# Performance work log

Hardware: AMD Instinct MI355X
Metric: run time of the kernel (lower is better)

## Reference

```python
import jax, jax.numpy as jnp
import numpy as np


def setup_inputs() -> dict:
    key = jax.random.key(0)
    ks = jax.random.split(key, 4)
    B, T, D, H = 128, 512, 256, 512
    scale = 1.0 / np.sqrt(D)
    return {
        "x": jax.random.normal(ks[0], (B, T, D), dtype=jnp.float32),
        "h0": jnp.zeros((B, H), dtype=jnp.float32),
        "kernelr": jax.random.normal(ks[1], (D, H), dtype=jnp.float32) * scale,
        "kernelz": jax.random.normal(ks[2], (D, H), dtype=jnp.float32) * scale,
        "kernelh": jax.random.normal(ks[3], (D, H), dtype=jnp.float32) * scale,
        "memoryr": jnp.ones((H,), dtype=jnp.float32),
        "memoryz": jnp.ones((H,), dtype=jnp.float32),
        "br": jnp.zeros((H,), dtype=jnp.float32),
        "bz": jnp.zeros((H,), dtype=jnp.float32),
    }


def reference(x, h0, kernelr, kernelz, kernelh, memoryr, memoryz, br, bz):
    # Precompute all input projections as one batched GEMM over (B*T, D).
    # xr/xz/xh: [T, B, H]
    xr = jnp.einsum("btd,dh->tbh", x, kernelr) + br
    xz = jnp.einsum("btd,dh->tbh", x, kernelz) + bz
    xh = jnp.einsum("btd,dh->tbh", x, kernelh)

    def step(h, inp):
        pr, pz, ph = inp
        r = jnp.tanh(pr + h * memoryr) + 1.0
        z = jax.nn.sigmoid(pz + h * memoryz)
        out = z * h + (1.0 - z) * jnp.tanh(ph + r * h)
        return out, out

    _, outs = jax.lax.scan(step, h0, (xr, xz, xh))  # outs: [T, B, H]
    return jnp.transpose(outs, (1, 0, 2))  # [B, T, H]
```

## Files before the change

kernel.cpp:

```cpp
#include <hip/hip_runtime.h>

typedef _Float16 f16;
typedef _Float16 f16x8 __attribute__((ext_vector_type(8)));
typedef _Float16 f16x4 __attribute__((ext_vector_type(4)));
typedef float f32x4 __attribute__((ext_vector_type(4)));

__device__ __forceinline__ float rcpf(float x) { return __builtin_amdgcn_rcpf(x); }

__global__ void __launch_bounds__(256) cvt_w(const float* __restrict__ Wr,
                                             const float* __restrict__ Wz,
                                             const float* __restrict__ Wh,
                                             f16* __restrict__ out) {
  int o = blockIdx.x * 256 + threadIdx.x;
  int rl = o & 15, ni = (o >> 4) & 3, kq = (o >> 6) & 3, kt = (o >> 8) & 7;
  int wnt = o >> 11;
  int w = wnt % 3, nt = wnt / 3;
  int n = nt * 64 + ni * 16 + rl;
  int k0 = kt * 32 + kq * 8;
  const float* W = (w == 0) ? Wr : ((w == 1) ? Wz : Wh);
  f16x8 v;
#pragma unroll
  for (int e = 0; e < 8; ++e) v[e] = (f16)W[(size_t)(k0 + e) * 512 + n];
  *(f16x8*)(out + (size_t)o * 8) = v;
}

__global__ void __launch_bounds__(256) cvt_x(const float* __restrict__ in,
                                             f16* __restrict__ out) {
  int o = blockIdx.x * 256 + threadIdx.x;
  int rl = o & 15, kq = (o >> 4) & 3, kt = (o >> 6) & 7, m16 = o >> 9;
  const float* src = in + (size_t)(m16 * 16 + rl) * 256 + kt * 32 + kq * 8;
  f16x8 v;
#pragma unroll
  for (int e = 0; e < 8; ++e) v[e] = (f16)src[e];
  *(f16x8*)(out + (size_t)o * 8) = v;
}

__global__ void __launch_bounds__(512, 4) brc_fused(
    const f16* __restrict__ Af, const f16* __restrict__ Bf,
    const float* __restrict__ h0, const float* __restrict__ mr,
    const float* __restrict__ mz, const float* __restrict__ br,
    const float* __restrict__ bz, float* __restrict__ out) {
  __shared__ __align__(16) f16 Pl[2][12288];
  const int tid = threadIdx.x;
  const int wid = tid >> 6, lane = tid & 63;
  const int bid = blockIdx.x;
  const int lid = (bid & 7) * 64 + (bid >> 3);
  const int b = lid >> 2, hs = lid & 3;

  const int w3 = wid >> 1, hh = wid & 1;
  const int nt = hs * 2 + hh;
  const char* Ap = (const char*)Af + lane * 16;
  const char* Bp = (const char*)Bf + (lane >> 4) * 1024 + (lane & 15) * 16;
  const int col = lane & 15, rbase = (lane >> 4) * 4;

  const int c = tid & 127;
  const int hg = hs * 128 + c;
  float h = h0[(size_t)b * 512 + hg];
  const float mrc = 2.0f * mr[hg], mzc = -mz[hg];
  const float br2 = 2.0f * br[hg], nbz = -bz[hg];

  auto gemm_phase = [&](int q) {
    f16* Pb = Pl[q & 1];
    f32x4 acc[2][4] = {};
#pragma unroll
    for (int kt = 0; kt < 8; ++kt) {
      f16x8 a[2], bfr[4];
#pragma unroll
      for (int mi = 0; mi < 2; ++mi)
        a[mi] = *(const f16x8*)(Ap +
                 (size_t)((b * 32 + q * 2 + mi) * 8 + kt) * 1024);
#pragma unroll
      for (int ni = 0; ni < 4; ++ni)
        bfr[ni] = *(const f16x8*)(Bp +
                   (size_t)((nt * 3 + w3) * 8 + kt) * 4096 + ni * 256);
#pragma unroll
      for (int mi = 0; mi < 2; ++mi)
#pragma unroll
        for (int ni = 0; ni < 4; ++ni)
          acc[mi][ni] = __builtin_amdgcn_mfma_f32_16x16x32_f16(
              a[mi], bfr[ni], acc[mi][ni], 0, 0, 0);
    }
#pragma unroll
    for (int mi = 0; mi < 2; ++mi) {
      int tl = mi * 16 + rbase;
#pragma unroll
      for (int ni = 0; ni < 4; ++ni) {
        int hl = hh * 64 + ni * 16 + col;
        f16x4 v;
#pragma unroll
        for (int r = 0; r < 4; ++r) v[r] = (f16)acc[mi][ni][r];
        *(f16x4*)&Pb[w3 * 4096 + (tl >> 3) * 1024 + hl * 8 + (tl & 7)] = v;
      }
    }
  };

  if (wid < 6) gemm_phase(0);

  for (int p = 0; p < 16; ++p) {
    __syncthreads();
    if (wid < 6) {
      if (p + 1 < 16) gemm_phase(p + 1);
    } else {
      const f16* Pr_ = &Pl[p & 1][c * 8];
      const f16* Pz_ = Pr_ + 4096;
      const f16* Ph_ = Pr_ + 8192;
      float* opm = out + ((size_t)b * 512 + p * 32) * 512 + hg;
#pragma unroll
      for (int g = 0; g < 4; ++g) {
        f16x8 R  = *(const f16x8*)(Pr_ + g * 1024);
        f16x8 Z  = *(const f16x8*)(Pz_ + g * 1024);
        f16x8 Hh = *(const f16x8*)(Ph_ + g * 1024);
#pragma unroll
        for (int j = 0; j < 8; ++j) {
          float prs = fmaf((float)R[j], 2.0f, br2);
          float pzs = fmaf((float)Z[j], -1.0f, nbz);
          float ph2 = (float)Hh[j] * 2.0f;
          float er = __expf(fmaf(h, mrc, prs));
          float rr = fmaf(-2.0f, rcpf(er + 1.0f), 2.0f);
          float ez = __expf(fmaf(h, mzc, pzs));
          float zz = rcpf(1.0f + ez);
          float ec = __expf(fmaf(rr, h + h, ph2));
          float cd = fmaf(-2.0f, rcpf(ec + 1.0f), 1.0f);
          h = fmaf(zz, h - cd, cd);
          __builtin_nontemporal_store(h, opm + (size_t)(g * 8 + j) * 512);
        }
      }
    }
  }
}

extern "C" void kernel_launch(void* const* d_in, const int* in_sizes, int n_in,
                              void* d_out, int out_size, void* d_ws, size_t ws_size,
                              hipStream_t stream) {
  const float* x  = (const float*)d_in[0];
  const float* h0 = (const float*)d_in[1];
  const float* kr = (const float*)d_in[2];
  const float* kz = (const float*)d_in[3];
  const float* kh = (const float*)d_in[4];
  const float* mr = (const float*)d_in[5];
  const float* mz = (const float*)d_in[6];
  const float* br = (const float*)d_in[7];
  const float* bz = (const float*)d_in[8];
  float* out = (float*)d_out;

  f16* Bf = (f16*)d_ws;
  f16* Xf = Bf + 393216;

  cvt_w<<<192, 256, 0, stream>>>(kr, kz, kh, Bf);
  cvt_x<<<8192, 256, 0, stream>>>(x, Xf);
  brc_fused<<<512, 512, 0, stream>>>(Xf, Bf, h0, mr, mz, br, bz, out);
}
```

Before: 116.5 us.

## Split fused GRU blocks into 64-column slices with one scan wave and larger time tiles

Each block now owns 64 hidden columns instead of 128, doubling the grid to 1024 blocks of 256 threads. Three GEMM waves each compute one gate over a 64-timestep by 64-column tile, and a single wave runs the recurrence over 64 timesteps per phase, which halves the number of phases and barriers. The intent is more parallel blocks and fewer synchronisations per sequence. The cost is that each recurrence wave walks a longer serial chain per phase and GEMM waves hold more accumulators per thread.

```diff
diff --git a/kernel.cpp b/kernel.cpp
--- a/kernel.cpp
+++ b/kernel.cpp
@@ -35,7 +35,7 @@
   *(f16x8*)(out + (size_t)o * 8) = v;
 }
 
-__global__ void __launch_bounds__(512, 4) brc_fused(
+__global__ void __launch_bounds__(256) brc_fused(
     const f16* __restrict__ Af, const f16* __restrict__ Bf,
     const float* __restrict__ h0, const float* __restrict__ mr,
     const float* __restrict__ mz, const float* __restrict__ br,
@@ -44,72 +44,71 @@
   const int tid = threadIdx.x;
   const int wid = tid >> 6, lane = tid & 63;
   const int bid = blockIdx.x;
-  const int lid = (bid & 7) * 64 + (bid >> 3);
-  const int b = lid >> 2, hs = lid & 3;
+  const int lid = (bid & 7) * 128 + (bid >> 3);
+  const int b = lid >> 3, hs = lid & 7;
 
-  const int w3 = wid >> 1, hh = wid & 1;
-  const int nt = hs * 2 + hh;
+  const int w3 = wid < 3 ? wid : 0;
   const char* Ap = (const char*)Af + lane * 16;
-  const char* Bp = (const char*)Bf + (lane >> 4) * 1024 + (lane & 15) * 16;
+  const char* Bp = (const char*)Bf + (lane >> 4) * 1024 + (lane & 15) * 16 +
+                   (size_t)(hs * 3 + w3) * 32768;
   const int col = lane & 15, rbase = (lane >> 4) * 4;
 
-  const int c = tid & 127;
-  const int hg = hs * 128 + c;
-  float h = h0[(size_t)b * 512 + hg];
-  const float mrc = 2.0f * mr[hg], mzc = -mz[hg];
-  const float br2 = 2.0f * br[hg], nbz = -bz[hg];
+  float h = 0.f, mrc = 0.f, mzc = 0.f, br2 = 0.f, nbz = 0.f;
+  if (wid == 3) {
+    int hg = hs * 64 + lane;
+    h = h0[(size_t)b * 512 + hg];
+    mrc = 2.0f * mr[hg]; mzc = -mz[hg];
+    br2 = 2.0f * br[hg]; nbz = -bz[hg];
+  }
 
   auto gemm_phase = [&](int q) {
     f16* Pb = Pl[q & 1];
-    f32x4 acc[2][4] = {};
+    f32x4 acc[4][4] = {};
 #pragma unroll
     for (int kt = 0; kt < 8; ++kt) {
-      f16x8 a[2], bfr[4];
+      f16x8 a[4], bf[4];
 #pragma unroll
-      for (int mi = 0; mi < 2; ++mi)
+      for (int mi = 0; mi < 4; ++mi)
         a[mi] = *(const f16x8*)(Ap +
-                 (size_t)((b * 32 + q * 2 + mi) * 8 + kt) * 1024);
+                 (size_t)((b * 32 + q * 4 + mi) * 8 + kt) * 1024);
 #pragma unroll
       for (int ni = 0; ni < 4; ++ni)
-        bfr[ni] = *(const f16x8*)(Bp +
-                   (size_t)((nt * 3 + w3) * 8 + kt) * 4096 + ni * 256);
+        bf[ni] = *(const f16x8*)(Bp + (size_t)kt * 4096 + ni * 256);
 #pragma unroll
-      for (int mi = 0; mi < 2; ++mi)
+      for (int mi = 0; mi < 4; ++mi)
 #pragma unroll
         for (int ni = 0; ni < 4; ++ni)
           acc[mi][ni] = __builtin_amdgcn_mfma_f32_16x16x32_f16(
-              a[mi], bfr[ni], acc[mi][ni], 0, 0, 0);
+              a[mi], bf[ni], acc[mi][ni], 0, 0, 0);
     }
 #pragma unroll
-    for (int mi = 0; mi < 2; ++mi) {
+    for (int mi = 0; mi < 4; ++mi) {
       int tl = mi * 16 + rbase;
 #pragma unroll
       for (int ni = 0; ni < 4; ++ni) {
-        int hl = hh * 64 + ni * 16 + col;
+        int hl = ni * 16 + col;
         f16x4 v;
 #pragma unroll
         for (int r = 0; r < 4; ++r) v[r] = (f16)acc[mi][ni][r];
-        *(f16x4*)&Pb[w3 * 4096 + (tl >> 3) * 1024 + hl * 8 + (tl & 7)] = v;
+        *(f16x4*)&Pb[w3 * 4096 + (tl >> 3) * 512 + hl * 8 + (tl & 7)] = v;
       }
     }
   };
 
-  if (wid < 6) gemm_phase(0);
+  if (wid < 3) gemm_phase(0);
 
-  for (int p = 0; p < 16; ++p) {
+  for (int p = 0; p < 8; ++p) {
     __syncthreads();
-    if (wid < 6) {
-      if (p + 1 < 16) gemm_phase(p + 1);
+    if (wid < 3) {
+      if (p + 1 < 8) gemm_phase(p + 1);
     } else {
-      const f16* Pr_ = &Pl[p & 1][c * 8];
-      const f16* Pz_ = Pr_ + 4096;
-      const f16* Ph_ = Pr_ + 8192;
-      float* opm = out + ((size_t)b * 512 + p * 32) * 512 + hg;
+      const f16* Pb = Pl[p & 1];
+      float* opm = out + ((size_t)b * 512 + p * 64) * 512 + hs * 64 + lane;
 #pragma unroll
-      for (int g = 0; g < 4; ++g) {
-        f16x8 R  = *(const f16x8*)(Pr_ + g * 1024);
-        f16x8 Z  = *(const f16x8*)(Pz_ + g * 1024);
-        f16x8 Hh = *(const f16x8*)(Ph_ + g * 1024);
+      for (int tg = 0; tg < 8; ++tg) {
+        f16x8 R  = *(const f16x8*)&Pb[tg * 512 + lane * 8];
+        f16x8 Z  = *(const f16x8*)&Pb[4096 + tg * 512 + lane * 8];
+        f16x8 Hh = *(const f16x8*)&Pb[8192 + tg * 512 + lane * 8];
 #pragma unroll
         for (int j = 0; j < 8; ++j) {
           float prs = fmaf((float)R[j], 2.0f, br2);
@@ -122,7 +121,7 @@
           float ec = __expf(fmaf(rr, h + h, ph2));
           float cd = fmaf(-2.0f, rcpf(ec + 1.0f), 1.0f);
           h = fmaf(zz, h - cd, cd);
-          __builtin_nontemporal_store(h, opm + (size_t)(g * 8 + j) * 512);
+          __builtin_nontemporal_store(h, opm + (size_t)(tg * 8 + j) * 512);
         }
       }
     }
@@ -148,5 +147,5 @@
 
   cvt_w<<<192, 256, 0, stream>>>(kr, kz, kh, Bf);
   cvt_x<<<8192, 256, 0, stream>>>(x, Xf);
-  brc_fused<<<512, 512, 0, stream>>>(Xf, Bf, h0, mr, mz, br, bz, out);
+  brc_fused<<<1024, 256, 0, stream>>>(Xf, Bf, h0, mr, mz, br, bz, out);
 }
```

Result: no change. 118.8 us (+2.0%).
